# Kernel optimization log

Measured on AMD Instinct MI355X. Metric: run time of the kernel, lower is better.

## Reference

```python
import jax, jax.numpy as jnp
import numpy as np
from jax import lax

N_IMG = 2
LEVEL_HW = [(200, 200), (100, 100), (50, 50), (25, 25), (13, 13)]
STRIDES = [4, 8, 16, 32, 64]
SIZES = [32.0, 64.0, 128.0, 256.0, 512.0]
A = 3
LEVEL_SIZES = [A * h * w for h, w in LEVEL_HW]
R = sum(LEVEL_SIZES)  # 159882
PRE_NMS = 1000   # pre_nms_top_n['testing']
POST_NMS = 1000  # post_nms_top_n['testing']
NMS_THRESH = 0.7
SCORE_THRESH = 0.0
MIN_SIZE = 1e-3
IMG_H = IMG_W = 800.0
BBOX_XFORM_CLIP = float(np.log(1000.0 / 16.0))


def _make_anchors():
    ratios = np.array([0.5, 1.0, 2.0])
    h_r = np.sqrt(ratios)
    w_r = 1.0 / h_r
    out = []
    for (h, w), stride, size in zip(LEVEL_HW, STRIDES, SIZES):
        ws = size * w_r
        hs = size * h_r
        base = np.stack([-ws / 2, -hs / 2, ws / 2, hs / 2], 1)  # [A,4]
        sx = (np.arange(w) + 0.5) * stride
        sy = (np.arange(h) + 0.5) * stride
        yy, xx = np.meshgrid(sy, sx, indexing='ij')
        shifts = np.stack([xx.ravel(), yy.ravel(), xx.ravel(), yy.ravel()], 1)  # [H*W,4]
        out.append((shifts[:, None, :] + base[None, :, :]).reshape(-1, 4))
    return np.concatenate(out, 0).astype(np.float32)  # [R,4]


def setup_inputs() -> dict:
    key = jax.random.key(0)
    k1, k2 = jax.random.split(key)
    objectness = jax.random.normal(k1, (N_IMG, R), jnp.float32)
    deltas = jax.random.normal(k2, (N_IMG, R, 4), jnp.float32) * 0.2
    anchors = jnp.asarray(_make_anchors())
    return {"objectness": objectness, "deltas": deltas, "anchors": anchors}


def _decode(deltas, anchors):
    # BoxCoder.decode with weights (1,1,1,1)
    wa = anchors[:, 2] - anchors[:, 0]
    ha = anchors[:, 3] - anchors[:, 1]
    cxa = anchors[:, 0] + 0.5 * wa
    cya = anchors[:, 1] + 0.5 * ha
    dx, dy, dw, dh = deltas[..., 0], deltas[..., 1], deltas[..., 2], deltas[..., 3]
    dw = jnp.minimum(dw, BBOX_XFORM_CLIP)
    dh = jnp.minimum(dh, BBOX_XFORM_CLIP)
    cx = dx * wa + cxa
    cy = dy * ha + cya
    w = jnp.exp(dw) * wa
    h = jnp.exp(dh) * ha
    return jnp.stack([cx - 0.5 * w, cy - 0.5 * h, cx + 0.5 * w, cy + 0.5 * h], -1)


def _nms_single(boxes, scores, lvl, valid):
    # batched_nms via per-level coordinate offset trick
    offs = lvl.astype(boxes.dtype) * (max(IMG_H, IMG_W) + 1.0)
    ob = boxes + offs[:, None]
    s = jnp.where(valid, scores, -1.0)
    order = jnp.argsort(-s)
    b = ob[order]          # offset boxes, score-descending
    raw = boxes[order]     # original boxes
    v = valid[order]
    ss = s[order]
    area = (b[:, 2] - b[:, 0]) * (b[:, 3] - b[:, 1])
    lt = jnp.maximum(b[:, None, :2], b[None, :, :2])
    rb = jnp.minimum(b[:, None, 2:], b[None, :, 2:])
    wh = jnp.clip(rb - lt, 0.0)
    inter = wh[..., 0] * wh[..., 1]
    iou = inter / (area[:, None] + area[None, :] - inter + 1e-9)  # [K,K]
    K = b.shape[0]

    def body(keep, i):
        suppressed = jnp.any(keep & (iou[:, i] > NMS_THRESH))
        keep = keep.at[i].set(v[i] & ~suppressed)
        return keep, None

    keep, _ = lax.scan(body, jnp.zeros((K,), bool), jnp.arange(K))
    # compact kept boxes (score order preserved) into fixed POST_NMS slots
    pos = jnp.where(keep, jnp.minimum(jnp.cumsum(keep) - 1, POST_NMS), POST_NMS)
    out_b = jnp.zeros((POST_NMS + 1, 4), boxes.dtype).at[pos].set(raw)[:POST_NMS]
    out_s = jnp.full((POST_NMS + 1,), -1.0, boxes.dtype).at[pos].set(ss)[:POST_NMS]
    return out_b, out_s


def _forward(objectness, deltas, anchors):
    proposals = _decode(deltas, anchors)  # [N,R,4]
    # per-level topk (pre_nms_top_n)
    idxs = []
    off = 0
    for n in LEVEL_SIZES:
        k = min(PRE_NMS, n)
        _, ti = lax.top_k(objectness[:, off:off + n], k)
        idxs.append(ti + off)
        off += n
    top_idx = jnp.concatenate(idxs, 1)  # [N,K]
    obj = jnp.take_along_axis(objectness, top_idx, 1)
    boxes = jnp.take_along_axis(proposals, top_idx[..., None], 1)
    levels = jnp.concatenate([jnp.full((n,), i, jnp.int32) for i, n in enumerate(LEVEL_SIZES)])
    lvl = levels[top_idx]
    scores = jax.nn.sigmoid(obj)
    # clip_boxes_to_image
    x1 = jnp.clip(boxes[..., 0], 0.0, IMG_W)
    y1 = jnp.clip(boxes[..., 1], 0.0, IMG_H)
    x2 = jnp.clip(boxes[..., 2], 0.0, IMG_W)
    y2 = jnp.clip(boxes[..., 3], 0.0, IMG_H)
    boxes = jnp.stack([x1, y1, x2, y2], -1)
    # remove_small_boxes + score_thresh -> validity mask (fixed shapes)
    valid = (x2 - x1 >= MIN_SIZE) & (y2 - y1 >= MIN_SIZE) & (scores >= SCORE_THRESH)
    return jax.vmap(_nms_single)(boxes, scores, lvl, valid)


def reference(objectness, deltas, anchors):
    return _forward(objectness, deltas, anchors)
```

## Files before the change

kernel.cpp:

```cpp
#include <hip/hip_runtime.h>

typedef unsigned long long u64;
typedef unsigned int u32;

#define R_TOT 159882
#define POST 1000
#define IMG_SZ 800.0f
#define NMS_TH 0.7f
#define BBOX_CLIP 4.135166556742356f
#define LCAP 1024

__device__ __forceinline__ float fadd_(float a, float b){ return __fadd_rn(a,b); }
__device__ __forceinline__ float fsub_(float a, float b){ return __fsub_rn(a,b); }
__device__ __forceinline__ float fmul_(float a, float b){ return __fmul_rn(a,b); }

__device__ __forceinline__ int lvl_len(int l){ const int L[5]={120000,30000,7500,1875,507}; return L[l]; }
__device__ __forceinline__ int lvl_off(int l){ const int L[5]={0,120000,150000,157500,159375}; return L[l]; }
__device__ __forceinline__ int lvl_k(int l){ const int L[5]={1000,1000,1000,1000,507}; return L[l]; }

__device__ __forceinline__ u32 mono_(u32 u){ return (u & 0x80000000u) ? ~u : (u | 0x80000000u); }

__device__ __forceinline__ u64 readlane64(u64 v, int i){
  u32 lo = (u32)__builtin_amdgcn_readlane((int)(u32)v, i);
  u32 hi = (u32)__builtin_amdgcn_readlane((int)(u32)(v >> 32), i);
  return ((u64)hi << 32) | (u64)lo;
}

__global__ __launch_bounds__(256) void k_front(const float* __restrict__ obj,
                                               int* histS,
                                               u64* mainS, u64* tieS,
                                               int* cntS, int* cnt2S){
  int g = blockIdx.x, sl = blockIdx.y;
  int img = g/5, lvl = g%5;
  int n = lvl_len(lvl), s0 = lvl_off(lvl), k = lvl_k(lvl);
  int tid = threadIdx.x, lane = tid & 63, wid = tid >> 6;
  __shared__ __align__(16) int lh[4096];
  __shared__ int wsum[4];
  __shared__ int sh_bs, lc, lc2;
  for (int i = tid; i < 4096; i += 256) lh[i] = 0;
  __syncthreads();
  int lo = (int)((long long)n * sl / 16), hiS = (int)((long long)n * (sl+1) / 16);
  int ns = hiS - lo;
  int ks = k < ns ? k : ns;
  const float* p = obj + img*R_TOT + s0;
  #pragma unroll 4
  for (int e = lo + tid; e < hiS; e += 256){
    u32 mu = mono_(__float_as_uint(p[e]));
    atomicAdd(&lh[(~mu) >> 20], 1);
  }
  __syncthreads();
  {
    int* dst = histS + (g*16 + sl)*4096;
    for (int i = tid; i < 4096; i += 256) dst[i] = lh[i];
  }
  int h[16];
  #pragma unroll
  for (int j = 0; j < 16; j++) h[j] = lh[16*tid + j];
  int part = 0;
  #pragma unroll
  for (int j = 0; j < 16; j++) part += h[j];
  int x = part;
  for (int d = 1; d < 64; d <<= 1){ int y = __shfl_up(x, d); if (lane >= d) x += y; }
  if (lane == 63) wsum[wid] = x;
  if (tid == 0){ lc = 0; lc2 = 0; }
  __syncthreads();
  int add = 0;
  for (int w = 0; w < wid; w++) add += wsum[w];
  int incl = x + add, excl = incl - part;
  if (excl < ks && ks <= incl){
    int cum = excl;
    #pragma unroll
    for (int q = 0; q < 16; q++){
      if (cum + h[q] >= ks){ sh_bs = 16*tid + q; break; }
      cum += h[q];
    }
  }
  __syncthreads();
  int bs = sh_bs;
  u64* lmain = (u64*)lh;
  u64* ltie  = (u64*)lh + 1024;
  #pragma unroll 4
  for (int e = lo + tid; e < hiS; e += 256){
    u32 mu = mono_(__float_as_uint(p[e]));
    u64 key56 = (((u64)(~mu)) << 24) | (u32)(s0 + e);
    int bin = (int)(key56 >> 44);
    if (bin < bs){ int pos = atomicAdd(&lc, 1); lmain[pos] = key56; }
    else if (bin == bs){ int pos = atomicAdd(&lc2, 1); if (pos < 1024) ltie[pos] = key56; }
  }
  __syncthreads();
  int idx16 = g*16 + sl;
  if (tid == 0){ cntS[idx16] = lc; cnt2S[idx16] = lc2; }
  for (int i = tid; i < lc; i += 256) mainS[idx16*1024 + i] = lmain[i];
  int c2l = lc2 < 1024 ? lc2 : 1024;
  for (int i = tid; i < c2l; i += 256) tieS[idx16*1024 + i] = ltie[i];
}

__global__ __launch_bounds__(1024) void k_seldecode(const float* __restrict__ obj,
                                                    const float4* __restrict__ deltas,
                                                    const float4* __restrict__ anchors,
                                                    const int* __restrict__ histS,
                                                    const u64* __restrict__ mainS,
                                                    const u64* __restrict__ tieS,
                                                    const int* __restrict__ cntS,
                                                    const int* __restrict__ cnt2S,
                                                    float4* boxL, float* scoreL,
                                                    float4* nbox, u64* okeyN, int* ncnt){
  int g = blockIdx.x, img = g/5, lvl = g%5;
  int s0 = lvl_off(lvl), n = lvl_len(lvl), k = lvl_k(lvl);
  const float* p = obj + img*R_TOT + s0;
  __shared__ u64 Lbuf[LCAP];
  __shared__ u64 mainL[1024];
  __shared__ __align__(16) float4 lbox[1024];
  __shared__ u64 lokey[1024];
  __shared__ unsigned char lval[1024];
  __shared__ int h16[16];
  __shared__ int scnt[16], tcnt[16];
  __shared__ int wsum16[16];
  __shared__ int sh_bs, sh_rem, sh_mc, sh_tc, sh_sc, sh_rem2, sh_ovf;
  __shared__ int sh_bs2, sh_rem2b, sh_c3;
  __shared__ u64 sh_thr;
  int tid = threadIdx.x, lane = tid & 63, wid = tid >> 6;
  if (tid < 16){ scnt[tid] = cntS[g*16 + tid]; tcnt[tid] = cnt2S[g*16 + tid]; }
  mainL[tid] = ~0ull;
  __syncthreads();
  if (tid == 0){
    int o = 0;
    #pragma unroll
    for (int q = 0; q < 16; q++) if (tcnt[q] > 1024) o = 1;
    sh_ovf = o; sh_mc = 0; sh_tc = 0; sh_sc = 0; sh_c3 = 0;
  }
  int h0 = 0, h1 = 0, h2 = 0, h3 = 0;
  {
    const int* hb = histS + g*16*4096 + 4*tid;
    #pragma unroll
    for (int s2 = 0; s2 < 16; s2++){
      int4 a = *(const int4*)(hb + s2*4096);
      h0 += a.x; h1 += a.y; h2 += a.z; h3 += a.w;
    }
  }
  int part = h0 + h1 + h2 + h3;
  int x = part;
  for (int d = 1; d < 64; d <<= 1){ int y = __shfl_up(x, d); if (lane >= d) x += y; }
  if (lane == 63) wsum16[wid] = x;
  __syncthreads();
  int add = 0;
  for (int w = 0; w < wid; w++) add += wsum16[w];
  int incl = x + add, excl = incl - part;
  if (excl < k && k <= incl){
    int cum = excl;
    if (cum + h0 >= k){ sh_bs = 4*tid;   sh_rem = k - cum; }
    else { cum += h0;
      if (cum + h1 >= k){ sh_bs = 4*tid+1; sh_rem = k - cum; }
      else { cum += h1;
        if (cum + h2 >= k){ sh_bs = 4*tid+2; sh_rem = k - cum; }
        else { cum += h2;    sh_bs = 4*tid+3; sh_rem = k - cum; }
      }
    }
  }
  __syncthreads();
  int bs = sh_bs;
  if (!sh_ovf){
    int mc = scnt[wid];
    int tcc = tcnt[wid] < 1024 ? tcnt[wid] : 1024;
    const u64* msrc = mainS + ((size_t)(g*16 + wid))*1024;
    const u64* tsrc = tieS + ((size_t)(g*16 + wid))*1024;
    for (int base = 0; base < mc; base += 256){
      int i0 = base + lane;
      u64 v0 = msrc[(i0       < mc) ? i0       : 0];
      u64 v1 = msrc[(i0+64    < mc) ? i0+64    : 0];
      u64 v2 = msrc[(i0+128   < mc) ? i0+128   : 0];
      u64 v3 = msrc[(i0+192   < mc) ? i0+192   : 0];
      #define PUSH(cond, vv) if (cond){ int b_ = (int)((vv) >> 44); \
        if (b_ < bs){ int pos = atomicAdd(&sh_mc, 1); mainL[pos] = (vv); } \
        else if (b_ == bs){ int pos = atomicAdd(&sh_tc, 1); if (pos < LCAP) Lbuf[pos] = (vv); } }
      PUSH(i0 < mc, v0) PUSH(i0+64 < mc, v1) PUSH(i0+128 < mc, v2) PUSH(i0+192 < mc, v3)
    }
    for (int base = 0; base < tcc; base += 256){
      int i0 = base + lane;
      u64 v0 = tsrc[(i0       < tcc) ? i0       : 0];
      u64 v1 = tsrc[(i0+64    < tcc) ? i0+64    : 0];
      u64 v2 = tsrc[(i0+128   < tcc) ? i0+128   : 0];
      u64 v3 = tsrc[(i0+192   < tcc) ? i0+192   : 0];
      PUSH(i0 < tcc, v0) PUSH(i0+64 < tcc, v1) PUSH(i0+128 < tcc, v2) PUSH(i0+192 < tcc, v3)
      #undef PUSH
    }
    __syncthreads();
    int nb = sh_mc, c2r = sh_tc, rem = sh_rem;
    if (c2r <= LCAP){
      int* chist = (int*)lbox;
      for (int i = tid; i < 4096; i += 1024) chist[i] = 0;
      __syncthreads();
      for (int e = tid; e < c2r; e += 1024){
        u64 kk = Lbuf[e];
        atomicAdd(&chist[(int)((kk >> 32) & 0xFFFu)], 1);
      }
      __syncthreads();
      int t0 = chist[4*tid], t1 = chist[4*tid+1], t2 = chist[4*tid+2], t3 = chist[4*tid+3];
      int tpart = t0 + t1 + t2 + t3;
      int tx = tpart;
      for (int d = 1; d < 64; d <<= 1){ int y = __shfl_up(tx, d); if (lane >= d) tx += y; }
      if (lane == 63) wsum16[wid] = tx;
      __syncthreads();
      int tadd = 0;
      for (int w = 0; w < wid; w++) tadd += wsum16[w];
      int tincl = tx + tadd, texcl = tincl - tpart;
      if (texcl < rem && rem <= tincl){
        int cum = texcl;
        if (cum + t0 >= rem){ sh_bs2 = 4*tid;   sh_rem2b = rem - cum; }
        else { cum += t0;
          if (cum + t1 >= rem){ sh_bs2 = 4*tid+1; sh_rem2b = rem - cum; }
          else { cum += t1;
            if (cum + t2 >= rem){ sh_bs2 = 4*tid+2; sh_rem2b = rem - cum; }
            else { cum += t2;    sh_bs2 = 4*tid+3; sh_rem2b = rem - cum; }
          }
        }
      }
      __syncthreads();
      int bs2 = sh_bs2;
      u64* subT = lokey;
      for (int e = tid; e < c2r; e += 1024){
        u64 kk = Lbuf[e];
        int sb2 = (int)((kk >> 32) & 0xFFFu);
        if (sb2 < bs2){ int p2 = atomicAdd(&sh_sc, 1); mainL[nb + p2] = kk; }
        else if (sb2 == bs2){ int p3 = atomicAdd(&sh_c3, 1); subT[p3] = kk; }
      }
      __syncthreads();
      int c3 = sh_c3, rem2b = sh_rem2b;
      for (int e = tid; e < c3; e += 1024){
        u64 kk = subT[e];
        int rk = 0;
        for (int qq = 0; qq < c3; qq++) rk += (subT[qq] < kk) ? 1 : 0;
        if (rk < rem2b){ int p2 = atomicAdd(&sh_sc, 1); mainL[nb + p2] = kk; }
      }
    } else {
      if (tid == 0) sh_ovf = 1;
    }
    __syncthreads();
  }
  if (sh_ovf){
    int* fh = (int*)lbox;
    for (int i = tid; i < 4096; i += 1024) fh[i] = 0;
    if (tid == 0){ sh_mc = 0; sh_sc = 0; }
    __syncthreads();
    for (int e = tid; e < n; e += 1024){
      u32 mu = mono_(__float_as_uint(p[e]));
      atomicAdd(&fh[(int)((~mu) >> 20)], 1);
    }
    __syncthreads();
    int f0 = fh[4*tid], f1 = fh[4*tid+1], f2 = fh[4*tid+2], f3 = fh[4*tid+3];
    int fpart = f0 + f1 + f2 + f3;
    int fx = fpart;
    for (int d = 1; d < 64; d <<= 1){ int y = __shfl_up(fx, d); if (lane >= d) fx += y; }
    if (lane == 63) wsum16[wid] = fx;
    __syncthreads();
    int fadd2 = 0;
    for (int w = 0; w < wid; w++) fadd2 += wsum16[w];
    int fincl = fx + fadd2, fexcl = fincl - fpart;
    if (fexcl < k && k <= fincl){
      int cum = fexcl;
      if (cum + f0 >= k){ sh_bs = 4*tid;   sh_rem = k - cum; }
      else { cum += f0;
        if (cum + f1 >= k){ sh_bs = 4*tid+1; sh_rem = k - cum; }
        else { cum += f1;
          if (cum + f2 >= k){ sh_bs = 4*tid+2; sh_rem = k - cum; }
          else { cum += f2;    sh_bs = 4*tid+3; sh_rem = k - cum; }
        }
      }
    }
    mainL[tid] = ~0ull;
    __syncthreads();
    int fbs = sh_bs;
    for (int e = tid; e < n; e += 1024){
      u32 mu = mono_(__float_as_uint(p[e]));
      u64 kk = (((u64)(~mu)) << 24) | (u32)(s0 + e);
      if ((int)(kk >> 44) < fbs){ int pos = atomicAdd(&sh_mc, 1); mainL[pos] = kk; }
    }
    __syncthreads();
    int nb = sh_mc;
    if (tid == 0){ sh_thr = ((u64)fbs) << 44; sh_rem2 = sh_rem; }
    __syncthreads();
    for (int shift = 40; shift >= 0; shift -= 4){
      if (tid < 16) h16[tid] = 0;
      __syncthreads();
      u64 pref = sh_thr;
      u64 himask = ~((1ull << (shift+4)) - 1ull);
      for (int e = tid; e < n; e += 1024){
        u32 mu = mono_(__float_as_uint(p[e]));
        u64 kk = (((u64)(~mu)) << 24) | (u32)(s0 + e);
        if ((kk & himask) == (pref & himask)) atomicAdd(&h16[(int)((kk >> shift) & 15)], 1);
      }
      __syncthreads();
      if (tid == 0){
        int r2 = sh_rem2, cum = 0;
        for (int d = 0; d < 16; d++){
          int hb2 = h16[d];
          if (cum + hb2 >= r2){ sh_thr = pref | ((u64)d << shift); sh_rem2 = r2 - cum; break; }
          cum += hb2;
        }
      }
      __syncthreads();
    }
    u64 thr = sh_thr;
    for (int e = tid; e < n; e += 1024){
      u32 mu = mono_(__float_as_uint(p[e]));
      u64 kk = (((u64)(~mu)) << 24) | (u32)(s0 + e);
      if ((int)(kk >> 44) == fbs && kk <= thr){ int p2 = atomicAdd(&sh_sc, 1); mainL[nb + p2] = kk; }
    }
    __syncthreads();
  }
  {
    volatile u64* vmain = mainL;
    for (int k2 = 2; k2 <= 1024; k2 <<= 1){
      for (int j = k2 >> 1; j > 0; j >>= 1){
        if (j >= 64 || (j == 32 && k2 >= 128)) __syncthreads();
        int i = tid, ixj = i ^ j;
        if (ixj > i){
          u64 a = vmain[i], b = vmain[ixj];
          bool up = (i & k2) == 0;
          if ((a > b) == up){ vmain[i] = b; vmain[ixj] = a; }
        }
      }
    }
  }
  __syncthreads();
  int r = tid, t = g*1024 + r;
  if (r < k){
    int idx = (int)(mainL[r] & 0xFFFFFFu);
    float4 a = anchors[idx];
    float4 d = deltas[img*R_TOT + idx];
    float o = obj[img*R_TOT + idx];
    float wa = fsub_(a.z, a.x), ha = fsub_(a.w, a.y);
    float cxa = fadd_(a.x, fmul_(0.5f, wa)), cya = fadd_(a.y, fmul_(0.5f, ha));
    float dw = fminf(d.z, BBOX_CLIP), dh = fminf(d.w, BBOX_CLIP);
    float cx = fadd_(fmul_(d.x, wa), cxa), cy = fadd_(fmul_(d.y, ha), cya);
    float w  = fmul_(expf(dw), wa),        h  = fmul_(expf(dh), ha);
    float x1 = fsub_(cx, fmul_(0.5f, w)), y1 = fsub_(cy, fmul_(0.5f, h));
    float x2 = fadd_(cx, fmul_(0.5f, w)), y2 = fadd_(cy, fmul_(0.5f, h));
    x1 = fminf(fmaxf(x1, 0.0f), IMG_SZ); y1 = fminf(fmaxf(y1, 0.0f), IMG_SZ);
    x2 = fminf(fmaxf(x2, 0.0f), IMG_SZ); y2 = fminf(fmaxf(y2, 0.0f), IMG_SZ);
    bool valid = (fsub_(x2, x1) >= 1e-3f) && (fsub_(y2, y1) >= 1e-3f);
    float e = expf(-o);
    float sig = __fdiv_rn(1.0f, fadd_(1.0f, e));
    float s = valid ? sig : -1.0f;
    u32 sb = __float_as_uint(s);
    u32 ms = (sb & 0x80000000u) ? ~sb : (sb | 0x80000000u);
    float4 b4 = make_float4(x1, y1, x2, y2);
    boxL[t] = b4;
    scoreL[t] = sig;
    lokey[r] = (((u64)(~ms)) << 32) | (u32)(lvl*1000 + r);
    lbox[r] = b4;
    lval[r] = valid ? 1 : 0;
  } else {
    lval[r] = 0;
  }
  __syncthreads();
  if (tid < 64){
    int cnt = 0;
    float off = (float)lvl * 801.0f;
    for (int base = 0; base < k; base += 64){
      int r2 = base + lane;
      bool v = (r2 < k) && lval[r2];
      float4 b = lbox[r2 < k ? r2 : 0];
      u64 mask = __ballot(v);
      int before = __popcll(mask & ((1ull << lane) - 1ull));
      if (v){
        int pos = cnt + before;
        nbox[g*1024 + pos] = make_float4(fadd_(b.x,off), fadd_(b.y,off), fadd_(b.z,off), fadd_(b.w,off));
        okeyN[g*1024 + pos] = lokey[r2];
      }
      cnt += __popcll(mask);
    }
    if (lane == 0) ncnt[g] = cnt;
  }
}

__global__ __launch_bounds__(64) void k_mask(const float4* __restrict__ nbox,
                                             const int* __restrict__ ncnt,
                                             u64* LTG2){
  int g = blockIdx.x, tr = blockIdx.y, tw = blockIdx.z;
  if (tw > tr) return;
  int m = ncnt[g];
  if (tr*64 >= m) return;
  __shared__ float4 shb[64];
  __shared__ float sharea[64];
  int lane = threadIdx.x;
  if (tw*64 + lane < m){
    float4 b = nbox[g*1024 + tw*64 + lane];
    shb[lane] = b;
    sharea[lane] = fmul_(fsub_(b.z,b.x), fsub_(b.w,b.y));
  }
  __syncthreads();
  int j = tr*64 + lane;
  if (j >= m) return;
  float4 a = nbox[g*1024 + j];
  float areaA = fmul_(fsub_(a.z,a.x), fsub_(a.w,a.y));
  int imax = m - tw*64; if (imax > 64) imax = 64;
  if (tw == tr){
    u64 bitsF = 0;
    for (int ii = lane+1; ii < imax; ii++){
      float4 b = shb[ii];
      float ltx = fmaxf(a.x, b.x), lty = fmaxf(a.y, b.y);
      float rbx = fminf(a.z, b.z), rby = fminf(a.w, b.w);
      float wx = fmaxf(fsub_(rbx, ltx), 0.0f), wy = fmaxf(fsub_(rby, lty), 0.0f);
      float inter = fmul_(wx, wy);
      float den = fadd_(fsub_(fadd_(areaA, sharea[ii]), inter), 1e-9f);
      if (__fdiv_rn(inter, den) > NMS_TH) bitsF |= (1ull << ii);
    }
    LTG2[((size_t)(g*1024 + j))*16 + 15] = bitsF;
  } else {
    u64 bits = 0;
    for (int ii = 0; ii < imax; ii++){
      float4 b = shb[ii];
      float ltx = fmaxf(a.x, b.x), lty = fmaxf(a.y, b.y);
      float rbx = fminf(a.z, b.z), rby = fminf(a.w, b.w);
      float wx = fmaxf(fsub_(rbx, ltx), 0.0f), wy = fmaxf(fsub_(rby, lty), 0.0f);
      float inter = fmul_(wx, wy);
      float den = fadd_(fsub_(fadd_(areaA, sharea[ii]), inter), 1e-9f);
      if (__fdiv_rn(inter, den) > NMS_TH) bits |= (1ull << ii);
    }
    LTG2[((size_t)(g*1024 + j))*16 + tw] = bits;
  }
}

struct ChunkBuf {
  ulonglong2 v0, v1, v2, v3, v4, v5, v6, v7;
  u64 ok;
};

__device__ __forceinline__ void issue_chunk(const u64* __restrict__ LT2,
                                            const u64* __restrict__ oK,
                                            int c, int lane, ChunkBuf& b){
  int row = c*64 + lane;
  const ulonglong2* rp = (const ulonglong2*)(LT2 + (size_t)row*16);
  b.v0 = rp[0]; b.v1 = rp[1]; b.v2 = rp[2]; b.v3 = rp[3];
  b.v4 = rp[4]; b.v5 = rp[5]; b.v6 = rp[6]; b.v7 = rp[7];
  b.ok = oK[row];
}

__device__ __forceinline__ void consume_chunk(const ChunkBuf& b, int c, int m, int lane,
                                              u64* KwR, u64* runsL, int& cnt){
  int row = c*64 + lane;
  bool inr = row < m;
  u64 supp = 0;
  #define TERM(q, val) supp |= (((q) < c) ? (val) : 0ull) & KwR[q];
  TERM(0,  b.v0.x) TERM(1,  b.v0.y) TERM(2,  b.v1.x) TERM(3,  b.v1.y)
  TERM(4,  b.v2.x) TERM(5,  b.v2.y) TERM(6,  b.v3.x) TERM(7,  b.v3.y)
  TERM(8,  b.v4.x) TERM(9,  b.v4.y) TERM(10, b.v5.x) TERM(11, b.v5.y)
  TERM(12, b.v6.x) TERM(13, b.v6.y) TERM(14, b.v7.x)
  #undef TERM
  u64 fwd = inr ? b.v7.y : 0;
  u64 live = __ballot(inr && (supp == 0));
  u64 fz = __ballot(fwd != 0);
  u64 kept = 0;
  while (1){
    u64 lf = live & fz;
    if (!lf){ kept |= live; break; }
    int i = __builtin_ctzll(lf);
    u64 bi = 1ull << i;
    u64 below = live & (bi - 1ull);
    kept |= below | bi;
    live &= ~(below | bi);
    live &= ~readlane64(fwd, i);
  }
  KwR[c] = kept;
  bool kp = (kept >> lane) & 1ull;
  int before = __popcll(kept & ((1ull << lane) - 1ull));
  if (kp) runsL[cnt + before] = b.ok;
  cnt += __popcll(kept);
}

__global__ __launch_bounds__(1024) void k_scanmerge(const u64* __restrict__ LTG2,
                                                    const int* __restrict__ ncnt,
                                                    const u64* __restrict__ okeyN,
                                                    const float4* __restrict__ boxL,
                                                    const float* __restrict__ scoreL,
                                                    float* out){
  int img = blockIdx.x, tid = threadIdx.x, lane = tid & 63, wid = tid >> 6;
  __shared__ u64 runs[5*1024];
  __shared__ u64 Kw[5][16];
  __shared__ int cl[5];
  if (wid < 5){
    int l = wid, g = img*5 + l;
    int m = ncnt[g];
    int nch = (m + 63) >> 6;
    const u64* LT2 = LTG2 + ((size_t)g*1024)*16;
    const u64* oK = okeyN + g*1024;
    u64* KwR = &Kw[l][0];
    u64* runsL = &runs[l*1024];
    int cnt = 0;
    ChunkBuf A, B;
    if (nch > 0){
      issue_chunk(LT2, oK, 0, lane, A);
      int c = 0;
      while (c < nch){
        if (c+1 < nch) issue_chunk(LT2, oK, c+1, lane, B);
        consume_chunk(A, c, m, lane, KwR, runsL, cnt);
        c++;
        if (c >= nch) break;
        if (c+1 < nch) issue_chunk(LT2, oK, c+1, lane, A);
        consume_chunk(B, c, m, lane, KwR, runsL, cnt);
        c++;
      }
    }
    if (lane == 0) cl[l] = cnt;
  } else {
    for (int t = tid - 320; t < POST; t += 704){
      out[img*POST*4 + t*4 + 0] = 0.0f;
      out[img*POST*4 + t*4 + 1] = 0.0f;
      out[img*POST*4 + t*4 + 2] = 0.0f;
      out[img*POST*4 + t*4 + 3] = 0.0f;
      out[2*POST*4 + img*POST + t] = -1.0f;
    }
  }
  __syncthreads();
  for (int idx = tid; idx < 5*1024; idx += 1024){
    int l = idx >> 10, i = idx & 1023;
    if (i < cl[l]){
      u64 key = runs[l*1024 + i];
      int o0 = l+1; if (o0 >= 5) o0 -= 5;
      int o1 = l+2; if (o1 >= 5) o1 -= 5;
      int o2 = l+3; if (o2 >= 5) o2 -= 5;
      int o3 = l+4; if (o3 >= 5) o3 -= 5;
      const u64* r0 = runs + (o0 << 10);
      const u64* r1 = runs + (o1 << 10);
      const u64* r2 = runs + (o2 << 10);
      const u64* r3 = runs + (o3 << 10);
      int lo0 = 0, hi0 = cl[o0];
      int lo1 = 0, hi1 = cl[o1];
      int lo2 = 0, hi2 = cl[o2];
      int lo3 = 0, hi3 = cl[o3];
      #pragma unroll 1
      for (int st = 0; st < 11; st++){
        int m0 = (lo0+hi0)>>1, m1 = (lo1+hi1)>>1, m2 = (lo2+hi2)>>1, m3 = (lo3+hi3)>>1;
        u64 a0 = r0[m0], a1 = r1[m1], a2 = r2[m2], a3 = r3[m3];
        if (lo0 < hi0){ if (a0 < key) lo0 = m0+1; else hi0 = m0; }
        if (lo1 < hi1){ if (a1 < key) lo1 = m1+1; else hi1 = m1; }
        if (lo2 < hi2){ if (a2 < key) lo2 = m2+1; else hi2 = m2; }
        if (lo3 < hi3){ if (a3 < key) lo3 = m3+1; else hi3 = m3; }
      }
      int rank = i + lo0 + lo1 + lo2 + lo3;
      if (rank < POST){
        int pos = (int)(key & 0xFFFFFFFFull);
        int lvl = pos / 1000, r = pos - lvl*1000;
        int gg = img*5 + lvl;
        float4 bo = boxL[gg*1024 + r];
        float sc = scoreL[gg*1024 + r];
        out[img*POST*4 + rank*4 + 0] = bo.x;
        out[img*POST*4 + rank*4 + 1] = bo.y;
        out[img*POST*4 + rank*4 + 2] = bo.z;
        out[img*POST*4 + rank*4 + 3] = bo.w;
        out[2*POST*4 + img*POST + rank] = sc;
      }
    }
  }
}

extern "C" void kernel_launch(void* const* d_in, const int* in_sizes, int n_in,
                              void* d_out, int out_size, void* d_ws, size_t ws_size,
                              hipStream_t stream){
  (void)in_sizes; (void)n_in; (void)out_size; (void)ws_size;
  const float*  obj     = (const float*)d_in[0];
  const float4* deltas  = (const float4*)d_in[1];
  const float4* anchors = (const float4*)d_in[2];
  float* out = (float*)d_out;
  char* ws = (char*)d_ws;
  int* histS   = (int*)(ws + 0);
  u64* mainS   = (u64*)(ws + 2621440);
  u64* tieS    = (u64*)(ws + 3932160);
  int* cntS    = (int*)(ws + 5242880);
  int* cnt2S   = (int*)(ws + 5243520);
  float4* boxL = (float4*)(ws + 5244160);
  float* scoreL= (float*)(ws + 5408000);
  u64* okeyN   = (u64*)(ws + 5448960);
  float4* nbox = (float4*)(ws + 5530880);
  u64* LTG2    = (u64*)(ws + 5694720);
  int* ncnt    = (int*)(ws + 7005440);

  {
    dim3 gf(10, 16);
    k_front<<<gf, 256, 0, stream>>>(obj, histS, mainS, tieS, cntS, cnt2S);
  }
  k_seldecode<<<10, 1024, 0, stream>>>(obj, deltas, anchors, histS, mainS, tieS, cntS, cnt2S,
                                       boxL, scoreL, nbox, okeyN, ncnt);
  {
    dim3 gm(10, 16, 16);
    k_mask<<<gm, 64, 0, stream>>>(nbox, ncnt, LTG2);
  }
  k_scanmerge<<<2, 1024, 0, stream>>>(LTG2, ncnt, okeyN, boxL, scoreL, out);
}
```

Baseline: 166.6 us.

## Split selection-decode kernel into separate select and sort/decode kernels

Splits the combined top-k selection and decode kernel into two launches. The first selects candidate keys and writes them to a global buffer; the second reloads them, bitonic-sorts them and decodes the boxes. This lowers the shared-memory footprint and register pressure of each kernel but adds a kernel launch and a global round trip. The sort also drops the volatile wavefront-synchronous shortcut and now calls __syncthreads on every step, which adds barriers.

Measured after the change: 154.3 us. -7.4%, faster.

```diff
diff --git a/kernel.cpp b/kernel.cpp
--- a/kernel.cpp
+++ b/kernel.cpp
@@ -95,24 +95,20 @@
   for (int i = tid; i < c2l; i += 256) tieS[idx16*1024 + i] = ltie[i];
 }
 
-__global__ __launch_bounds__(1024) void k_seldecode(const float* __restrict__ obj,
-                                                    const float4* __restrict__ deltas,
-                                                    const float4* __restrict__ anchors,
-                                                    const int* __restrict__ histS,
-                                                    const u64* __restrict__ mainS,
-                                                    const u64* __restrict__ tieS,
-                                                    const int* __restrict__ cntS,
-                                                    const int* __restrict__ cnt2S,
-                                                    float4* boxL, float* scoreL,
-                                                    float4* nbox, u64* okeyN, int* ncnt){
+__global__ __launch_bounds__(1024) void k_selA(const float* __restrict__ obj,
+                                               const int* __restrict__ histS,
+                                               const u64* __restrict__ mainS,
+                                               const u64* __restrict__ tieS,
+                                               const int* __restrict__ cntS,
+                                               const int* __restrict__ cnt2S,
+                                               u64* selG){
   int g = blockIdx.x, img = g/5, lvl = g%5;
   int s0 = lvl_off(lvl), n = lvl_len(lvl), k = lvl_k(lvl);
   const float* p = obj + img*R_TOT + s0;
   __shared__ u64 Lbuf[LCAP];
   __shared__ u64 mainL[1024];
-  __shared__ __align__(16) float4 lbox[1024];
-  __shared__ u64 lokey[1024];
-  __shared__ unsigned char lval[1024];
+  __shared__ __align__(16) int chist[4096];
+  __shared__ u64 subT[1024];
   __shared__ int h16[16];
   __shared__ int scnt[16], tcnt[16];
   __shared__ int wsum16[16];
@@ -187,7 +183,6 @@
     __syncthreads();
     int nb = sh_mc, c2r = sh_tc, rem = sh_rem;
     if (c2r <= LCAP){
-      int* chist = (int*)lbox;
       for (int i = tid; i < 4096; i += 1024) chist[i] = 0;
       __syncthreads();
       for (int e = tid; e < c2r; e += 1024){
@@ -217,7 +212,6 @@
       }
       __syncthreads();
       int bs2 = sh_bs2;
-      u64* subT = lokey;
       for (int e = tid; e < c2r; e += 1024){
         u64 kk = Lbuf[e];
         int sb2 = (int)((kk >> 32) & 0xFFFu);
@@ -238,16 +232,15 @@
     __syncthreads();
   }
   if (sh_ovf){
-    int* fh = (int*)lbox;
-    for (int i = tid; i < 4096; i += 1024) fh[i] = 0;
+    for (int i = tid; i < 4096; i += 1024) chist[i] = 0;
     if (tid == 0){ sh_mc = 0; sh_sc = 0; }
     __syncthreads();
     for (int e = tid; e < n; e += 1024){
       u32 mu = mono_(__float_as_uint(p[e]));
-      atomicAdd(&fh[(int)((~mu) >> 20)], 1);
-    }
-    __syncthreads();
-    int f0 = fh[4*tid], f1 = fh[4*tid+1], f2 = fh[4*tid+2], f3 = fh[4*tid+3];
+      atomicAdd(&chist[(int)((~mu) >> 20)], 1);
+    }
+    __syncthreads();
+    int f0 = chist[4*tid], f1 = chist[4*tid+1], f2 = chist[4*tid+2], f3 = chist[4*tid+3];
     int fpart = f0 + f1 + f2 + f3;
     int fx = fpart;
     for (int d = 1; d < 64; d <<= 1){ int y = __shfl_up(fx, d); if (lane >= d) fx += y; }
@@ -304,21 +297,36 @@
     for (int e = tid; e < n; e += 1024){
       u32 mu = mono_(__float_as_uint(p[e]));
       u64 kk = (((u64)(~mu)) << 24) | (u32)(s0 + e);
-      if ((int)(kk >> 44) == fbs && kk <= thr){ int p2 = atomicAdd(&sh_sc, 1); mainL[nb + p2] = kk; }
-    }
-    __syncthreads();
-  }
-  {
-    volatile u64* vmain = mainL;
-    for (int k2 = 2; k2 <= 1024; k2 <<= 1){
-      for (int j = k2 >> 1; j > 0; j >>= 1){
-        if (j >= 64 || (j == 32 && k2 >= 128)) __syncthreads();
-        int i = tid, ixj = i ^ j;
-        if (ixj > i){
-          u64 a = vmain[i], b = vmain[ixj];
-          bool up = (i & k2) == 0;
-          if ((a > b) == up){ vmain[i] = b; vmain[ixj] = a; }
-        }
+      if ((int)(kk >> 44) == sh_bs && kk <= thr){ int p2 = atomicAdd(&sh_sc, 1); mainL[nb + p2] = kk; }
+    }
+    __syncthreads();
+  }
+  selG[g*1024 + tid] = mainL[tid];
+}
+
+__global__ __launch_bounds__(1024) void k_selB(const float* __restrict__ obj,
+                                               const float4* __restrict__ deltas,
+                                               const float4* __restrict__ anchors,
+                                               const u64* __restrict__ selG,
+                                               float4* boxL, float* scoreL,
+                                               float4* nbox, u64* okeyN, int* ncnt){
+  int g = blockIdx.x, img = g/5, lvl = g%5;
+  int k = lvl_k(lvl);
+  __shared__ u64 mainL[1024];
+  __shared__ float4 lbox[1024];
+  __shared__ u64 lokey[1024];
+  __shared__ unsigned char lval[1024];
+  int tid = threadIdx.x, lane = tid & 63;
+  mainL[tid] = selG[g*1024 + tid];
+  __syncthreads();
+  for (int k2 = 2; k2 <= 1024; k2 <<= 1){
+    for (int j = k2 >> 1; j > 0; j >>= 1){
+      __syncthreads();
+      int i = tid, ixj = i ^ j;
+      if (ixj > i){
+        u64 a = mainL[i], b = mainL[ixj];
+        bool up = (i & k2) == 0;
+        if ((a > b) == up){ mainL[i] = b; mainL[ixj] = a; }
       }
     }
   }
@@ -575,13 +583,14 @@
   float4* nbox = (float4*)(ws + 5530880);
   u64* LTG2    = (u64*)(ws + 5694720);
   int* ncnt    = (int*)(ws + 7005440);
+  u64* selG    = (u64*)(ws + 7005504);
 
   {
     dim3 gf(10, 16);
     k_front<<<gf, 256, 0, stream>>>(obj, histS, mainS, tieS, cntS, cnt2S);
   }
-  k_seldecode<<<10, 1024, 0, stream>>>(obj, deltas, anchors, histS, mainS, tieS, cntS, cnt2S,
-                                       boxL, scoreL, nbox, okeyN, ncnt);
+  k_selA<<<10, 1024, 0, stream>>>(obj, histS, mainS, tieS, cntS, cnt2S, selG);
+  k_selB<<<10, 1024, 0, stream>>>(obj, deltas, anchors, selG, boxL, scoreL, nbox, okeyN, ncnt);
   {
     dim3 gm(10, 16, 16);
     k_mask<<<gm, 64, 0, stream>>>(nbox, ncnt, LTG2);
```
